# Performance work log

Hardware: AMD Instinct MI355X
Metric: run time of the kernel (lower is better)

The kernel has to match this reference:

```python
import jax, jax.numpy as jnp
import numpy as np

H = 16       # num_heads
BS = 256     # block_size
TOPK = 3     # top_k routed blocks


def setup_inputs() -> dict:
    rng = jax.random.key(0)
    ks = jax.random.split(rng, 11)
    B, S, D = 1, 2048, 2048
    w = 0.02  # weight init scale
    return {
        "query": jax.random.normal(ks[0], (B, S, D), jnp.float32),
        "key": jax.random.normal(ks[1], (B, S, D), jnp.float32),
        "value": jax.random.normal(ks[2], (B, S, D), jnp.float32),
        "Wq": jax.random.normal(ks[3], (D, D), jnp.float32) * w,
        "bq": jnp.zeros((D,), jnp.float32),
        "Wk": jax.random.normal(ks[4], (D, D), jnp.float32) * w,
        "bk": jnp.zeros((D,), jnp.float32),
        "Wv": jax.random.normal(ks[5], (D, D), jnp.float32) * w,
        "bv": jnp.zeros((D,), jnp.float32),
        "Wo": jax.random.normal(ks[6], (D, D), jnp.float32) * w,
        "bo": jnp.zeros((D,), jnp.float32),
    }


def reference(query, key, value, Wq, bq, Wk, bk, Wv, bv, Wo, bo):
    B, S, D = query.shape
    Dh = D // H
    Nb = S // BS
    scale = 1.0 / np.sqrt(Dh)

    def proj(x, W, b):
        return (x @ W.T + b).reshape(B, S, H, Dh).transpose(0, 2, 1, 3)  # [B,H,S,Dh]

    q = proj(query, Wq, bq)
    k = proj(key, Wk, bk)
    v = proj(value, Wv, bv)

    kb = k.reshape(B, H, Nb, BS, Dh)
    vb = v.reshape(B, H, Nb, BS, Dh)

    # --- MoBA routing: query vs per-block mean key (unscaled, as in source) ---
    k_mean = kb.mean(3)                                   # [B,H,Nb,Dh]
    route = jnp.einsum('bhsd,bhnd->bhsn', q, k_mean)      # [B,H,S,Nb]
    qblk = jnp.arange(S) // BS
    blk = jnp.arange(Nb)
    not_past = qblk[:, None] <= blk[None, :]              # current or future block
    route = jnp.where(not_past[None, None], -jnp.inf, route)
    keff = min(TOPK, Nb)
    _, idx = jax.lax.top_k(route, keff)                   # [B,H,S,K]
    sel = (jax.nn.one_hot(idx, Nb, dtype=jnp.float32).sum(-2) > 0)
    sel = sel & (~not_past)[None, None]                   # only strictly-past blocks kept

    # --- self attention: causal within each query's own block ---
    qb = q.reshape(B, H, Nb, BS, Dh)
    s_self = jnp.einsum('bhnqd,bhnkd->bhnqk', qb, kb) * scale
    causal = jnp.tril(jnp.ones((BS, BS), bool))
    s_self = jnp.where(causal, s_self, -jnp.inf)
    self_out = jnp.einsum('bhnqk,bhnkd->bhnqd',
                          jax.nn.softmax(s_self, -1), vb).reshape(B, H, S, Dh)

    # --- moba attention: softmax over union of selected past blocks (non-causal) ---
    key_mask = jnp.repeat(sel, BS, axis=-1)               # [B,H,S,S]
    s_moba = jnp.einsum('bhqd,bhkd->bhqk', q, k) * scale
    s_moba = jnp.where(key_mask, s_moba, -1e30)
    a = jax.nn.softmax(s_moba, -1)
    moba_out = jnp.einsum('bhqk,bhkd->bhqd', a, v)
    has_keys = key_mask.any(-1)[..., None]                # first block has none
    moba_out = jnp.where(has_keys, moba_out, 0.0)

    out = (self_out + moba_out).transpose(0, 2, 1, 3).reshape(B, S, D)
    return out @ Wo.T + bo
```

## Files before the change

### kernel.cpp

```cpp
#include <hip/hip_runtime.h>

#define NH 16
#define SEQ 2048
#define DIM 2048
#define DH 128
#define BSZ 256
#define NB 8

typedef _Float16 half8 __attribute__((ext_vector_type(8)));
typedef _Float16 half4 __attribute__((ext_vector_type(4)));
typedef float f32x4 __attribute__((ext_vector_type(4)));

typedef __attribute__((address_space(1))) void gvoid;
typedef __attribute__((address_space(3))) void lvoid;

__device__ __forceinline__ void gload_lds16(const void* g, void* l) {
  __builtin_amdgcn_global_load_lds((gvoid*)g, (lvoid*)l, 16, 0, 0);
}

__device__ __forceinline__ float ldf(const void* p, size_t i, int isbf) {
  if (isbf) {
    unsigned short u = ((const unsigned short*)p)[i];
    return __uint_as_float(((unsigned)u) << 16);
  }
  return ((const float*)p)[i];
}

__device__ __forceinline__ unsigned short f2bf(float x) {
  unsigned u = __float_as_uint(x);
  u += 0x7fffu + ((u >> 16) & 1u);
  return (unsigned short)(u >> 16);
}

__global__ void detect_kernel(const void* q, int* flag) {
  const int lane = threadIdx.x;
  const unsigned short* u = (const unsigned short*)q;
  int cnt = 0;
  for (int i = lane; i < 1024; i += 64) {
    int ex = (u[2 * i] >> 7) & 0xff;
    cnt += (ex >= 103 && ex <= 143) ? 1 : 0;
  }
  #pragma unroll
  for (int mk = 1; mk <= 32; mk <<= 1) cnt += __shfl_xor(cnt, mk);
  if (lane == 0) *flag = (cnt > 512) ? 1 : 0;
}

struct CvArgs {
  const void* in[7];
  _Float16* out[7];
};
__global__ __launch_bounds__(256) void tohalf_all(CvArgs c, const int* __restrict__ flagp) {
  const int isbf = flagp[0];
  const void* in = c.in[blockIdx.y];
  _Float16* out = c.out[blockIdx.y];
  size_t i0 = ((size_t)blockIdx.x * 256 + threadIdx.x) * 4;
  #pragma unroll
  for (int k = 0; k < 4; ++k) out[i0 + k] = (_Float16)ldf(in, i0 + k, isbf);
}

__global__ __launch_bounds__(256) void kbm_kernel(const void* __restrict__ key,
                                                  float* __restrict__ kbm,
                                                  const int* __restrict__ flagp) {
  __shared__ float red[2][128];
  const int dl = threadIdx.x & 127, hf = threadIdx.x >> 7;
  const int d = blockIdx.x * 128 + dl;
  const int n = blockIdx.y;
  const int isbf = flagp[0];
  float acc = 0.f;
  for (int r = 0; r < 128; ++r)
    acc += ldf(key, ((size_t)n * 256 + hf * 128 + r) * DIM + d, isbf);
  red[hf][dl] = acc;
  __syncthreads();
  if (hf == 0) kbm[n * DIM + d] = (red[0][dl] + red[1][dl]) * (1.f / 256.f);
}

__global__ __launch_bounds__(256) void kmean_kernel(const void* __restrict__ Wk,
                                                    const void* __restrict__ bk,
                                                    const float* __restrict__ kbm,
                                                    float* __restrict__ kmean,
                                                    const int* __restrict__ flagp) {
  const int wave = threadIdx.x >> 6, lane = threadIdx.x & 63;
  const int d = blockIdx.x * 4 + wave;
  const int isbf = flagp[0];
  float acc[8] = {0.f, 0.f, 0.f, 0.f, 0.f, 0.f, 0.f, 0.f};
  for (int it = 0; it < 32; ++it) {
    const int e = it * 64 + lane;
    const float wv = ldf(Wk, (size_t)d * DIM + e, isbf);
    #pragma unroll
    for (int n = 0; n < 8; ++n) acc[n] += wv * kbm[n * DIM + e];
  }
  #pragma unroll
  for (int n = 0; n < 8; ++n)
    #pragma unroll
    for (int mk = 1; mk <= 32; mk <<= 1) acc[n] += __shfl_xor(acc[n], mk);
  if (lane < 8) kmean[lane * DIM + d] = acc[lane] + ldf(bk, d, isbf);
}

__global__ __launch_bounds__(128) void routeR_kernel(const void* __restrict__ Wq,
                                                     const float* __restrict__ kmean,
                                                     float* __restrict__ Rt,
                                                     const int* __restrict__ flagp) {
  const int e = blockIdx.x * 128 + threadIdx.x;
  const int h = blockIdx.y;
  const int isbf = flagp[0];
  float acc[8] = {0.f, 0.f, 0.f, 0.f, 0.f, 0.f, 0.f, 0.f};
  for (int dh = 0; dh < DH; ++dh) {
    float wv = ldf(Wq, (size_t)(h * DH + dh) * DIM + e, isbf);
    #pragma unroll
    for (int n = 0; n < 8; ++n) acc[n] += wv * kmean[n * DIM + h * DH + dh];
  }
  #pragma unroll
  for (int n = 0; n < 8; ++n) Rt[(size_t)e * 128 + h * 8 + n] = acc[n];
}

__global__ void cbias_kernel(const void* __restrict__ bq, const float* __restrict__ kmean,
                             float* __restrict__ cb, const int* __restrict__ flagp) {
  const int hn = threadIdx.x;
  const int h = hn >> 3, n = hn & 7;
  const int isbf = flagp[0];
  float a = 0.f;
  for (int dh = 0; dh < DH; ++dh)
    a += ldf(bq, h * DH + dh, isbf) * kmean[n * DIM + h * DH + dh];
  cb[hn] = a;
}

__global__ __launch_bounds__(128) void route_topk_kernel(const void* __restrict__ query,
                                                         const float* __restrict__ Rt,
                                                         const float* __restrict__ cb,
                                                         unsigned int* __restrict__ sel,
                                                         const int* __restrict__ flagp) {
  __shared__ float qs[4][2048];
  __shared__ float rv[4][128];
  const int s0 = blockIdx.x * 4;
  const int tid = threadIdx.x;
  const int isbf = flagp[0];
  float* qsf = &qs[0][0];
  for (int i = tid; i < 4 * 2048; i += 128)
    qsf[i] = ldf(query, (size_t)s0 * DIM + i, isbf);
  __syncthreads();
  const int hn = tid;
  float a0 = 0.f, a1 = 0.f, a2 = 0.f, a3 = 0.f;
  for (int e = 0; e < DIM; ++e) {
    float r = Rt[(size_t)e * 128 + hn];
    a0 += r * qs[0][e];
    a1 += r * qs[1][e];
    a2 += r * qs[2][e];
    a3 += r * qs[3][e];
  }
  const float c = cb[hn];
  rv[0][hn] = a0 + c; rv[1][hn] = a1 + c; rv[2][hn] = a2 + c; rv[3][hn] = a3 + c;
  __syncthreads();
  if (tid < 64) {
    const int si = tid >> 4, h = tid & 15;
    const int s = s0 + si;
    const int qblk = s >> 8;
    unsigned picked = 0;
    for (int it = 0; it < 3; ++it) {
      float best = -__builtin_inff();
      int bi = -1;
      for (int n = 0; n < qblk; ++n) {
        if (picked & (1u << n)) continue;
        float v = rv[si][h * 8 + n];
        if (v > best) { best = v; bi = n; }
      }
      if (bi >= 0) picked |= (1u << bi);
    }
    sel[(size_t)h * SEQ + s] = picked;
  }
}

struct QkvArgs {
  const _Float16* A[3];
  const _Float16* B[3];
  const void* bias[3];
  _Float16* out[3];
};
__global__ __launch_bounds__(256) void gemm_qkv(QkvArgs ar, const int* __restrict__ flagp) {
  __shared__ _Float16 As[128 * 32];
  __shared__ _Float16 Bs[128 * 32];
  const int z = blockIdx.z;
  const _Float16* A = ar.A[z];
  const _Float16* B = ar.B[z];
  const void* bias = ar.bias[z];
  _Float16* out = ar.out[z];
  const int epi = (z == 2) ? 1 : 0;

  const int tid = threadIdx.x;
  const int lane = tid & 63;
  const int wave = tid >> 6;
  const int m0 = blockIdx.x * 128;
  const int n0 = blockIdx.y * 128;
  const int wm = (wave >> 1) * 64;
  const int wn = (wave & 1) * 64;
  const int lr = lane >> 2;
  const int lc = (lane & 3) * 8;
  const int qg = lane >> 4;
  const int cl = lane & 15;

  f32x4 acc[4][4] = {};

  for (int kt = 0; kt < 64; ++kt) {
    const int k0 = kt * 32;
    #pragma unroll
    for (int cc = 0; cc < 2; ++cc) {
      const int chunk = wave * 2 + cc;
      const int row = chunk * 16 + lr;
      gload_lds16(A + (size_t)(m0 + row) * DIM + k0 + lc, &As[chunk * 512]);
      gload_lds16(B + (size_t)(n0 + row) * DIM + k0 + lc, &Bs[chunk * 512]);
    }
    __syncthreads();
    half8 af[4], bf[4];
    #pragma unroll
    for (int mi = 0; mi < 4; ++mi)
      af[mi] = *(const half8*)&As[(wm + mi * 16 + cl) * 32 + qg * 8];
    #pragma unroll
    for (int ni = 0; ni < 4; ++ni)
      bf[ni] = *(const half8*)&Bs[(wn + ni * 16 + cl) * 32 + qg * 8];
    #pragma unroll
    for (int mi = 0; mi < 4; ++mi)
      #pragma unroll
      for (int ni = 0; ni < 4; ++ni)
        acc[mi][ni] = __builtin_amdgcn_mfma_f32_16x16x32_f16(af[mi], bf[ni], acc[mi][ni], 0, 0, 0);
    __syncthreads();
  }

  const int isbf = flagp[0];
  #pragma unroll
  for (int mi = 0; mi < 4; ++mi) {
    #pragma unroll
    for (int ni = 0; ni < 4; ++ni) {
      const int col = n0 + wn + ni * 16 + cl;
      const float bv = ldf(bias, col, isbf);
      const int h = col >> 7, dh = col & 127;
      const int row0 = m0 + wm + mi * 16 + qg * 4;
      if (epi == 0) {
        const int kk = dh >> 5, rem = dh & 31;
        #pragma unroll
        for (int r = 0; r < 4; ++r)
          out[((size_t)(h * 4 + kk) * SEQ + row0 + r) * 32 + rem] = (_Float16)(acc[mi][ni][r] + bv);
      } else {
        half4 pk;
        #pragma unroll
        for (int r = 0; r < 4; ++r) pk[r] = (_Float16)(acc[mi][ni][r] + bv);
        *(half4*)&out[((size_t)(h * 64 + (row0 >> 5)) * 128 + dh) * 32 + (row0 & 31)] = pk;
      }
    }
  }
}

__global__ __launch_bounds__(256) void gemm_out(const _Float16* __restrict__ A,
                                                const _Float16* __restrict__ B,
                                                const void* __restrict__ bias,
                                                void* __restrict__ out,
                                                const int* __restrict__ flagp) {
  __shared__ _Float16 As[128 * 32];
  __shared__ _Float16 Bs[64 * 32];
  const int tid = threadIdx.x;
  const int lane = tid & 63;
  const int wave = tid >> 6;
  const int m0 = blockIdx.x * 128;
  const int n0 = blockIdx.y * 64;
  const int wm = (wave >> 1) * 64;
  const int wn = (wave & 1) * 32;
  const int lr = lane >> 2;
  const int lc = (lane & 3) * 8;
  const int qg = lane >> 4;
  const int cl = lane & 15;

  f32x4 acc[4][2] = {};

  for (int kt = 0; kt < 64; ++kt) {
    const int k0 = kt * 32;
    #pragma unroll
    for (int cc = 0; cc < 2; ++cc) {
      const int chunk = wave * 2 + cc;
      const int row = chunk * 16 + lr;
      gload_lds16(A + (size_t)(m0 + row) * DIM + k0 + lc, &As[chunk * 512]);
    }
    {
      const int row = wave * 16 + lr;
      gload_lds16(B + (size_t)(n0 + row) * DIM + k0 + lc, &Bs[wave * 512]);
    }
    __syncthreads();
    half8 af[4], bf[2];
    #pragma unroll
    for (int mi = 0; mi < 4; ++mi)
      af[mi] = *(const half8*)&As[(wm + mi * 16 + cl) * 32 + qg * 8];
    #pragma unroll
    for (int ni = 0; ni < 2; ++ni)
      bf[ni] = *(const half8*)&Bs[(wn + ni * 16 + cl) * 32 + qg * 8];
    #pragma unroll
    for (int mi = 0; mi < 4; ++mi)
      #pragma unroll
      for (int ni = 0; ni < 2; ++ni)
        acc[mi][ni] = __builtin_amdgcn_mfma_f32_16x16x32_f16(af[mi], bf[ni], acc[mi][ni], 0, 0, 0);
    __syncthreads();
  }

  const int isbf = flagp[0];
  #pragma unroll
  for (int mi = 0; mi < 4; ++mi) {
    #pragma unroll
    for (int ni = 0; ni < 2; ++ni) {
      const int col = n0 + wn + ni * 16 + cl;
      const float bv = ldf(bias, col, isbf);
      #pragma unroll
      for (int r = 0; r < 4; ++r) {
        const int row = m0 + wm + mi * 16 + qg * 4 + r;
        const float v = acc[mi][ni][r] + bv;
        if (isbf) ((unsigned short*)out)[(size_t)row * DIM + col] = f2bf(v);
        else      ((float*)out)[(size_t)row * DIM + col] = v;
      }
    }
  }
}

#define PST 136
#define OST 132
__global__ __launch_bounds__(256, 3) void attn_kernel(const _Float16* __restrict__ qg_,
                                                      const _Float16* __restrict__ kg_,
                                                      const _Float16* __restrict__ vg_,
                                                      const unsigned int* __restrict__ sel,
                                                      _Float16* __restrict__ attn) {
  __shared__ float smemf[4 * 16 * OST + 4 * 16];
  const int tid = threadIdx.x;
  const int lane = tid & 63;
  const int w = tid >> 6;
  const int q16 = 127 - (blockIdx.x >> 4);
  const int h = blockIdx.x & 15;
  const int q0 = q16 * 16;
  const int nblk = q16 >> 4;
  const int qoff = (q16 & 15) * 16;
  const int qg = lane >> 4;
  const int cl = lane & 15;
  const float scale = 0.08838834764831845f;
  _Float16* myP = (_Float16*)(smemf + w * 16 * OST);
  float* myO = smemf + w * 16 * OST;
  float* ml = smemf + 4 * 16 * OST;

  half8 aq[4];
  #pragma unroll
  for (int kk = 0; kk < 4; ++kk)
    aq[kk] = *(const half8*)(qg_ + ((size_t)(h * 4 + kk) * SEQ + q0 + cl) * 32 + qg * 8);

  unsigned selr[4];
  #pragma unroll
  for (int r = 0; r < 4; ++r) selr[r] = sel[(size_t)h * SEQ + q0 + qg * 4 + r];
  unsigned un = selr[0] | selr[1] | selr[2] | selr[3];
  un |= __shfl_xor(un, 16);
  un |= __shfl_xor(un, 32);

  float psum[4] = {0.f, 0.f, 0.f, 0.f};
  f32x4 om[8] = {};

  auto process = [&](int blk, int c, bool is_self) {
    #pragma unroll
    for (int ct = 0; ct < 8; ++ct) {
      f32x4 a = {};
      const int key = blk * 256 + c * 128 + ct * 16 + cl;
      #pragma unroll
      for (int kk = 0; kk < 4; ++kk) {
        half8 bk = *(const half8*)(kg_ + ((size_t)(h * 4 + kk) * SEQ + key) * 32 + qg * 8);
        a = __builtin_amdgcn_mfma_f32_16x16x32_f16(aq[kk], bk, a, 0, 0, 0);
      }
      const int klocal = c * 128 + ct * 16 + cl;
      #pragma unroll
      for (int r = 0; r < 4; ++r) {
        const bool ok = is_self ? (klocal <= qoff + qg * 4 + r) : (bool)((selr[r] >> blk) & 1u);
        const float s = fminf(a[r] * scale, 11.f);
        const float p = ok ? __expf(s) : 0.f;
        psum[r] += p;
        myP[(qg * 4 + r) * PST + ct * 16 + cl] = (_Float16)p;
      }
    }
    asm volatile("s_waitcnt lgkmcnt(0)" ::: "memory");
    half8 ap[4];
    #pragma unroll
    for (int kk = 0; kk < 4; ++kk)
      ap[kk] = *(const half8*)&myP[cl * PST + kk * 32 + qg * 8];
    #pragma unroll
    for (int dt = 0; dt < 8; ++dt) {
      f32x4 a = om[dt];
      #pragma unroll
      for (int kk = 0; kk < 4; ++kk) {
        half8 bv = *(const half8*)(vg_ + ((size_t)(h * 64 + blk * 8 + c * 4 + kk) * 128 + dt * 16 + cl) * 32 + qg * 8);
        a = __builtin_amdgcn_mfma_f32_16x16x32_f16(ap[kk], bv, a, 0, 0, 0);
      }
      om[dt] = a;
    }
  };

  if (w == 0) {
    process(nblk, 0, true);
    process(nblk, 1, true);
  } else {
    int pos = 0;
    for (int j = 0; j < nblk; ++j) {
      if (!((un >> j) & 1u)) continue;
      if ((pos % 3) == (w - 1)) {
        process(j, 0, false);
        process(j, 1, false);
      }
      ++pos;
    }
  }

  #pragma unroll
  for (int r = 0; r < 4; ++r)
    #pragma unroll
    for (int mk = 1; mk <= 8; mk <<= 1) psum[r] += __shfl_xor(psum[r], mk);

  asm volatile("s_waitcnt lgkmcnt(0)" ::: "memory");
  #pragma unroll
  for (int dt = 0; dt < 8; ++dt)
    #pragma unroll
    for (int r = 0; r < 4; ++r)
      myO[(qg * 4 + r) * OST + dt * 16 + cl] = om[dt][r];
  if (cl == 0) {
    #pragma unroll
    for (int r = 0; r < 4; ++r) ml[w * 16 + qg * 4 + r] = psum[r];
  }
  __syncthreads();

  const float* O0 = smemf;
  const float* O1 = smemf + 16 * OST;
  const float* O2 = smemf + 2 * 16 * OST;
  const float* O3 = smemf + 3 * 16 * OST;
  #pragma unroll
  for (int r = 0; r < 4; ++r) {
    const int row = qg * 4 + r;
    const float l0 = ml[row];
    const float lmoba = ml[16 + row] + ml[32 + row] + ml[48 + row];
    const float inv0 = 1.f / l0;
    const float invm = (lmoba > 0.f) ? 1.f / lmoba : 0.f;
    #pragma unroll
    for (int d2 = 0; d2 < 2; ++d2) {
      const int dt = w * 2 + d2;
      const int idx = row * OST + dt * 16 + cl;
      const float o = O0[idx] * inv0 + (O1[idx] + O2[idx] + O3[idx]) * invm;
      attn[(size_t)(q0 + row) * DIM + h * DH + dt * 16 + cl] = (_Float16)o;
    }
  }
}

extern "C" void kernel_launch(void* const* d_in, const int* in_sizes, int n_in,
                              void* d_out, int out_size, void* d_ws, size_t ws_size,
                              hipStream_t stream) {
  (void)in_sizes; (void)n_in; (void)out_size; (void)ws_size;
  const void* query = d_in[0];
  const void* key   = d_in[1];
  const void* value = d_in[2];
  const void* Wq = d_in[3]; const void* bq = d_in[4];
  const void* Wk = d_in[5]; const void* bk = d_in[6];
  const void* Wv = d_in[7]; const void* bv = d_in[8];
  const void* Wo = d_in[9]; const void* bo = d_in[10];

  char* ws = (char*)d_ws;
  const size_t MB = 1024ull * 1024ull;
  _Float16* Xq   = (_Float16*)(ws + 0 * MB);
  _Float16* Xk   = (_Float16*)(ws + 8 * MB);
  _Float16* Xv   = (_Float16*)(ws + 16 * MB);
  _Float16* Wqh  = (_Float16*)(ws + 24 * MB);
  _Float16* Wkh  = (_Float16*)(ws + 32 * MB);
  _Float16* Wvh  = (_Float16*)(ws + 40 * MB);
  _Float16* Woh  = (_Float16*)(ws + 48 * MB);
  _Float16* Qg   = (_Float16*)(ws + 56 * MB);
  _Float16* Kg   = (_Float16*)(ws + 64 * MB);
  _Float16* Vg   = (_Float16*)(ws + 72 * MB);
  _Float16* atB  = (_Float16*)(ws + 80 * MB);
  float* kbm     = (float*)(ws + 88 * MB);
  float* kmean   = (float*)(ws + 88 * MB + 64 * 1024);
  float* Rt      = (float*)(ws + 88 * MB + 128 * 1024);
  float* cb      = (float*)(ws + 89 * MB + 128 * 1024);
  int*   flag    = (int*)(ws + 89 * MB + 132 * 1024);
  unsigned int* sel = (unsigned int*)(ws + 89 * MB + 136 * 1024);

  detect_kernel<<<1, 64, 0, stream>>>(query, flag);

  CvArgs cv;
  cv.in[0] = query; cv.out[0] = Xq;
  cv.in[1] = key;   cv.out[1] = Xk;
  cv.in[2] = value; cv.out[2] = Xv;
  cv.in[3] = Wq;    cv.out[3] = Wqh;
  cv.in[4] = Wk;    cv.out[4] = Wkh;
  cv.in[5] = Wv;    cv.out[5] = Wvh;
  cv.in[6] = Wo;    cv.out[6] = Woh;
  tohalf_all<<<dim3(4096, 7), 256, 0, stream>>>(cv, flag);

  kbm_kernel<<<dim3(16, 8), 256, 0, stream>>>(key, kbm, flag);
  kmean_kernel<<<512, 256, 0, stream>>>(Wk, bk, kbm, kmean, flag);
  routeR_kernel<<<dim3(16, 16), 128, 0, stream>>>(Wq, kmean, Rt, flag);
  cbias_kernel<<<1, 128, 0, stream>>>(bq, kmean, cb, flag);
  route_topk_kernel<<<512, 128, 0, stream>>>(query, Rt, cb, sel, flag);

  QkvArgs qa;
  qa.A[0] = Xq; qa.B[0] = Wqh; qa.bias[0] = bq; qa.out[0] = Qg;
  qa.A[1] = Xk; qa.B[1] = Wkh; qa.bias[1] = bk; qa.out[1] = Kg;
  qa.A[2] = Xv; qa.B[2] = Wvh; qa.bias[2] = bv; qa.out[2] = Vg;
  gemm_qkv<<<dim3(16, 16, 3), 256, 0, stream>>>(qa, flag);

  attn_kernel<<<2048, 256, 0, stream>>>(Qg, Kg, Vg, sel, atB);

  gemm_out<<<dim3(16, 32), 256, 0, stream>>>(atB, Woh, bo, d_out, flag);
}
```

Before: 514.6 us.

## Split routing score computation into split-K partial kernel and separate top-k pass

```diff
diff --git a/kernel.cpp b/kernel.cpp
--- a/kernel.cpp
+++ b/kernel.cpp
@@ -124,49 +124,60 @@
   cb[hn] = a;
 }
 
-__global__ __launch_bounds__(128) void route_topk_kernel(const void* __restrict__ query,
+__global__ __launch_bounds__(256) void route_part_kernel(const void* __restrict__ query,
                                                          const float* __restrict__ Rt,
-                                                         const float* __restrict__ cb,
-                                                         unsigned int* __restrict__ sel,
+                                                         float* __restrict__ part,
                                                          const int* __restrict__ flagp) {
-  __shared__ float qs[4][2048];
-  __shared__ float rv[4][128];
-  const int s0 = blockIdx.x * 4;
+  __shared__ float qs[256][8];
+  const int s0 = blockIdx.x * 8;
+  const int eh = blockIdx.y;
   const int tid = threadIdx.x;
-  const int isbf = flagp[0];
-  float* qsf = &qs[0][0];
-  for (int i = tid; i < 4 * 2048; i += 128)
-    qsf[i] = ldf(query, (size_t)s0 * DIM + i, isbf);
-  __syncthreads();
-  const int hn = tid;
-  float a0 = 0.f, a1 = 0.f, a2 = 0.f, a3 = 0.f;
-  for (int e = 0; e < DIM; ++e) {
-    float r = Rt[(size_t)e * 128 + hn];
-    a0 += r * qs[0][e];
-    a1 += r * qs[1][e];
-    a2 += r * qs[2][e];
-    a3 += r * qs[3][e];
-  }
-  const float c = cb[hn];
-  rv[0][hn] = a0 + c; rv[1][hn] = a1 + c; rv[2][hn] = a2 + c; rv[3][hn] = a3 + c;
-  __syncthreads();
-  if (tid < 64) {
-    const int si = tid >> 4, h = tid & 15;
-    const int s = s0 + si;
-    const int qblk = s >> 8;
-    unsigned picked = 0;
-    for (int it = 0; it < 3; ++it) {
-      float best = -__builtin_inff();
-      int bi = -1;
-      for (int n = 0; n < qblk; ++n) {
-        if (picked & (1u << n)) continue;
-        float v = rv[si][h * 8 + n];
-        if (v > best) { best = v; bi = n; }
-      }
-      if (bi >= 0) picked |= (1u << bi);
-    }
-    sel[(size_t)h * SEQ + s] = picked;
-  }
+  const int hn = tid & 127;
+  const int sh = tid >> 7;
+  const int isbf = flagp[0];
+  float acc[4] = {0.f, 0.f, 0.f, 0.f};
+
+  for (int ch = 0; ch < 4; ++ch) {
+    const int e0 = eh * 1024 + ch * 256;
+    __syncthreads();
+    #pragma unroll
+    for (int p = 0; p < 8; ++p)
+      qs[tid][p] = ldf(query, (size_t)(s0 + p) * DIM + e0 + tid, isbf);
+    __syncthreads();
+    for (int e = 0; e < 256; ++e) {
+      const float r = Rt[(size_t)(e0 + e) * 128 + hn];
+      const f32x4 q4 = *(const f32x4*)&qs[e][sh * 4];
+      #pragma unroll
+      for (int j = 0; j < 4; ++j) acc[j] += r * q4[j];
+    }
+  }
+  #pragma unroll
+  for (int j = 0; j < 4; ++j)
+    part[((size_t)eh * SEQ + s0 + sh * 4 + j) * 128 + hn] = acc[j];
+}
+
+__global__ __launch_bounds__(256) void route_topk2_kernel(const float* __restrict__ part,
+                                                          const float* __restrict__ cb,
+                                                          unsigned int* __restrict__ sel) {
+  const int item = blockIdx.x * 256 + threadIdx.x;
+  const int s = item >> 4, h = item & 15;
+  const int qblk = s >> 8;
+  float rv[8];
+  #pragma unroll
+  for (int n = 0; n < 8; ++n)
+    rv[n] = part[(size_t)s * 128 + h * 8 + n] +
+            part[((size_t)SEQ + s) * 128 + h * 8 + n] + cb[h * 8 + n];
+  unsigned picked = 0;
+  for (int it = 0; it < 3; ++it) {
+    float best = -__builtin_inff();
+    int bi = -1;
+    for (int n = 0; n < qblk; ++n) {
+      if (picked & (1u << n)) continue;
+      if (rv[n] > best) { best = rv[n]; bi = n; }
+    }
+    if (bi >= 0) picked |= (1u << bi);
+  }
+  sel[(size_t)h * SEQ + s] = picked;
 }
 
 struct QkvArgs {
@@ -468,6 +479,7 @@
   _Float16* Kg   = (_Float16*)(ws + 64 * MB);
   _Float16* Vg   = (_Float16*)(ws + 72 * MB);
   _Float16* atB  = (_Float16*)(ws + 80 * MB);
+  float* part    = (float*)(ws + 80 * MB);
   float* kbm     = (float*)(ws + 88 * MB);
   float* kmean   = (float*)(ws + 88 * MB + 64 * 1024);
   float* Rt      = (float*)(ws + 88 * MB + 128 * 1024);
@@ -491,7 +503,8 @@
   kmean_kernel<<<512, 256, 0, stream>>>(Wk, bk, kbm, kmean, flag);
   routeR_kernel<<<dim3(16, 16), 128, 0, stream>>>(Wq, kmean, Rt, flag);
   cbias_kernel<<<1, 128, 0, stream>>>(bq, kmean, cb, flag);
-  route_topk_kernel<<<512, 128, 0, stream>>>(query, Rt, cb, sel, flag);
+  route_part_kernel<<<dim3(256, 2), 256, 0, stream>>>(query, Rt, part, flag);
+  route_topk2_kernel<<<128, 256, 0, stream>>>(part, cb, sel);
 
   QkvArgs qa;
   qa.A[0] = Xq; qa.B[0] = Wqh; qa.bias[0] = bq; qa.out[0] = Qg;
```

New measurement: 471.7 us. -8.3%, faster.
